# Performance work log

Measured on AMD Instinct MI355X. Metric: run time of the kernel, lower is better.

Reference implementation:

```python
import jax, jax.numpy as jnp
import numpy as np

E = 100000   # number of edges
S = 64       # multiplicity of 0e (scalar) irreps
V = 32       # multiplicity of 1o (vector) irreps; also number of gates
RS3 = 1.0 / np.sqrt(3.0)   # wigner_3j constant for (1,1,0)/(0,1,1)/(1,0,1) paths
RS6 = 1.0 / np.sqrt(6.0)   # (unused here: no 1o output from 1o x 1o)

# per-path normalization: 1/sqrt(n_paths_to_slot * mul1 * mul2), e3nn-style 'uvw'
A_SS_S = (2.0 * S * S) ** -0.5
A_VV_S = (2.0 * V * V) ** -0.5 * RS3
A_SS_G = (2.0 * S * S) ** -0.5
A_VV_G = (2.0 * V * V) ** -0.5 * RS3
A_SV_V = (2.0 * S * V) ** -0.5 * RS3
A_VS_V = (2.0 * V * S) ** -0.5 * RS3


def setup_inputs() -> dict:
    key = jax.random.key(0)
    ks = jax.random.split(key, 12)
    d_in = S + 3 * V
    return {
        "fea_in1": jax.random.normal(ks[0], (E, d_in), jnp.float32),
        "fea_in2": jax.random.normal(ks[1], (E, d_in), jnp.float32),
        "fea_weight": jax.random.normal(ks[2], (E, V), jnp.float32),   # unused (kept for signature parity)
        "batch_edge": jax.random.randint(ks[3], (E,), 0, 16, jnp.int32),  # unused (norm='')
        # SeparateWeightTensorProduct ('uvw') weights, one tensor per CG path
        "w_ss_s": jax.random.normal(ks[4], (S, S, S), jnp.float32),  # 0e x 0e -> 0e (scalars)
        "w_vv_s": jax.random.normal(ks[5], (V, V, S), jnp.float32),  # 1o x 1o -> 0e (scalars)
        "w_ss_g": jax.random.normal(ks[6], (S, S, V), jnp.float32),  # 0e x 0e -> 0e (gates)
        "w_vv_g": jax.random.normal(ks[7], (V, V, V), jnp.float32),  # 1o x 1o -> 0e (gates)
        "w_sv_v": jax.random.normal(ks[8], (S, V, V), jnp.float32),  # 0e x 1o -> 1o
        "w_vs_v": jax.random.normal(ks[9], (V, S, V), jnp.float32),  # 1o x 0e -> 1o
        # equivariant o3.Linear weights (channel mixing per irrep, shared over m)
        "wl_s": jax.random.normal(ks[10], (S, S), jnp.float32),
        "wl_v": jax.random.normal(ks[11], (V, V), jnp.float32),
    }


def reference(fea_in1, fea_in2, fea_weight, batch_edge,
              w_ss_s, w_vv_s, w_ss_g, w_vv_g, w_sv_v, w_vs_v, wl_s, wl_v):
    # split flattened irreps features: [S scalars | V vectors * 3]
    s1 = fea_in1[:, :S]
    v1 = fea_in1[:, S:].reshape(-1, V, 3)
    s2 = fea_in2[:, :S]
    v2 = fea_in2[:, S:].reshape(-1, V, 3)

    # --- separate-weight tensor product (fully connected 'uvw' paths) ---
    z_s = (A_SS_S * jnp.einsum('uvw,eu,ev->ew', w_ss_s, s1, s2)
           + A_VV_S * jnp.einsum('uvw,eui,evi->ew', w_vv_s, v1, v2))   # (E,S) 0e
    z_g = (A_SS_G * jnp.einsum('uvw,eu,ev->ew', w_ss_g, s1, s2)
           + A_VV_G * jnp.einsum('uvw,eui,evi->ew', w_vv_g, v1, v2))   # (E,V) gates 0e
    z_v = (A_SV_V * jnp.einsum('uvw,eu,evi->ewi', w_sv_v, s1, v2)
           + A_VS_V * jnp.einsum('uvw,eui,ev->ewi', w_vs_v, v1, s2))   # (E,V,3) 1o

    # --- gated nonlinearity: silu on scalars, sigmoid gates on vectors ---
    s_act = jax.nn.silu(z_s)
    v_act = jax.nn.sigmoid(z_g)[:, :, None] * z_v

    # --- equivariant linear (per-irrep channel mixing, fan-in normalized) ---
    s_out = (s_act @ wl_s) * (S ** -0.5)                    # (E,S)
    v_out = jnp.einsum('evi,vw->ewi', v_act, wl_v) * (V ** -0.5)  # (E,V,3)

    return jnp.concatenate([s_out, v_out.reshape(-1, 3 * V)], axis=-1)  # (E, S+3V)
```

## Files before the change

kernel.cpp:

```cpp
#include <hip/hip_runtime.h>


typedef _Float16 f16;
typedef _Float16 f16x4 __attribute__((ext_vector_type(4)));
typedef _Float16 f16x8 __attribute__((ext_vector_type(8)));
typedef float    f32x4 __attribute__((ext_vector_type(4)));

constexpr float A_SS  = 0.011048543456039806f;
constexpr float A_VV  = 0.012757759747374832f;
constexpr float A_SV  = 0.009021097956087904f;
constexpr float SO_SC = 0.125f;
constexpr float VO_SC = 0.1767766952966369f;

#define MFMA16(A, B, C) __builtin_amdgcn_mfma_f32_16x16x32_f16((A), (B), (C), 0, 0, 0)

static __device__ __forceinline__ f16x8 splat8(f16 x) {
    return (f16x8){x, x, x, x, x, x, x, x};
}

__global__ void prep_weights(const float* __restrict__ wss_s, const float* __restrict__ wvv_s,
                             const float* __restrict__ wss_g, const float* __restrict__ wvv_g,
                             const float* __restrict__ wsv,   const float* __restrict__ wvs,
                             const float* __restrict__ wls,   const float* __restrict__ wlv,
                             f16* __restrict__ b1p, f16* __restrict__ b2p,
                             f16* __restrict__ wlsP, f16* __restrict__ wlvP)
{
    int idx = blockIdx.x * 256 + threadIdx.x;
    const int N1 = 2 * 160 * 3 * 512;
    const int N2 = 128 * 2 * 512;
    const int N3 = 8 * 512;
    const int N4 = 2 * 512;
    if (idx < N1) {
        int j = idx & 7, L = (idx >> 3) & 63, rest = idx >> 9;
        int t3 = rest % 3, rc = rest / 3;
        int c = rc % 160, nh2 = rc / 160;
        int k = c * 32 + (L >> 4) * 8 + j;
        int n = (nh2 * 3 + t3) * 16 + (L & 15);
        float val;
        if (k < 4096) { int u = k >> 6, v = k & 63, p = u * 64 + v;
            val = A_SS * (n < 64 ? wss_s[p * 64 + n] : wss_g[p * 32 + (n - 64)]);
        } else { int k2 = k - 4096; int u = k2 >> 5, v = k2 & 31, p = u * 32 + v;
            val = A_VV * (n < 64 ? wvv_s[p * 64 + n] : wvv_g[p * 32 + (n - 64)]);
        }
        b1p[idx] = (f16)val;
    } else if (idx < N1 + N2) {
        int id2 = idx - N1;
        int j = id2 & 7, L = (id2 >> 3) & 63, ct = id2 >> 9;
        int t = ct & 1, c = ct >> 1;
        int k = c * 32 + (L >> 4) * 8 + j;
        int n = t * 16 + (L & 15);
        float val;
        if (k < 2048) { int u = k >> 5, v = k & 31; val = wsv[(u * 32 + v) * 32 + n]; }
        else { int k2 = k - 2048; int u = k2 >> 6, v = k2 & 63; val = wvs[(u * 64 + v) * 32 + n]; }
        b2p[id2] = (f16)(A_SV * val);
    } else if (idx < N1 + N2 + N3) {
        int id3 = idx - N1 - N2;
        int j = id3 & 7, L = (id3 >> 3) & 63, ct = id3 >> 9;
        int t = ct & 3, kc = ct >> 2;
        int k = kc * 32 + (L >> 4) * 8 + j;
        int n = t * 16 + (L & 15);
        wlsP[id3] = (f16)(SO_SC * wls[k * 64 + n]);
    } else if (idx < N1 + N2 + N3 + N4) {
        int id4 = idx - N1 - N2 - N3;
        int j = id4 & 7, L = (id4 >> 3) & 63, t = id4 >> 9;
        int k = (L >> 4) * 8 + j;
        int n = t * 16 + (L & 15);
        wlvP[id4] = (f16)(VO_SC * wlv[k * 32 + n]);
    }
}

__global__ __launch_bounds__(256, 4)
void seconv_mfma(const float* __restrict__ fea1, const float* __restrict__ fea2,
                 const f16* __restrict__ b1p, const f16* __restrict__ b2p,
                 const f16* __restrict__ wlsP, const f16* __restrict__ wlvP,
                 float* __restrict__ out, int E)
{
    __shared__ __align__(128) char smem[40960];
    f16*   zSh  = (f16*)smem;
    f16*   zGh  = (f16*)(smem + 9216);
    f16*   ZVH  = (f16*)(smem + 13568);
    float* OUTV = (float*)smem;

    const int tid  = threadIdx.x;
    const int lane = tid & 63;
    const int m    = lane & 15;
    const int quad = lane >> 4;
    const int w    = tid >> 6;
    const int h    = w & 1;
    const int nh   = w >> 1;
    const int tb   = nh * 3;
    const int e0   = blockIdx.x * 64;

    auto ld8 = [&](int e, int hc) -> f16x8 {
        int b = (e * 640 + hc * 2) ^ ((e & 7) << 4);
        return *(const f16x8*)(smem + b);
    };
    auto ld4 = [&](int e, int hc) -> f16x4 {
        int b = (e * 640 + hc * 2) ^ ((e & 7) << 4);
        return *(const f16x4*)(smem + b);
    };
    auto st2 = [&](int e, int hc, f16 v) {
        int b = (e * 640 + hc * 2) ^ ((e & 7) << 4);
        *(f16*)(smem + b) = v;
    };

    for (int i = tid; i < 64 * 160; i += 256) {
        int e = i / 160, c = i - e * 160;
        int ge = e0 + e; if (ge >= E) ge = E - 1;
        float a = fea1[ge * 160 + c];
        float b = fea2[ge * 160 + c];
        if (c < 64) { st2(e, c, (f16)a); st2(e, 64 + c, (f16)b); }
        else { int c2 = c - 64; int v = c2 / 3, ii = c2 - v * 3;
               st2(e, 128 + ii * 32 + v, (f16)a);
               st2(e, 224 + ii * 32 + v, (f16)b); }
    }
    __syncthreads();

    const int eA = h * 32 + m;
    const int eB = h * 32 + 16 + m;

    f32x4 acc[2][3];
    #pragma unroll
    for (int p = 0; p < 2; ++p)
        #pragma unroll
        for (int t = 0; t < 3; ++t) acc[p][t] = (f32x4){0.f, 0.f, 0.f, 0.f};

    const f16* pB = b1p + __builtin_amdgcn_readfirstlane(nh) * (160 * 3 * 512);
    f32x4 bq[2][3];
    #pragma unroll
    for (int t = 0; t < 3; ++t) bq[0][t] = *(const f32x4*)(pB + t * 512 + lane * 8);
    pB += 1536;
    #pragma unroll
    for (int t = 0; t < 3; ++t) bq[1][t] = *(const f32x4*)(pB + t * 512 + lane * 8);
    pB += 1536;

    {
        f16x8 s2q[2][2];
        #pragma unroll
        for (int p = 0; p < 2; ++p)
            #pragma unroll
            for (int vh = 0; vh < 2; ++vh)
                s2q[p][vh] = ld8(p ? eB : eA, 64 + vh * 32 + quad * 8);

        for (int ub = 0; ub < 8; ++ub) {
            f16x8 s1Ab = ld8(eA, ub * 8);
            f16x8 s1Bb = ld8(eB, ub * 8);
            #pragma unroll
            for (int uj = 0; uj < 8; ++uj) {
                f16x8 s1A = splat8(s1Ab[uj]);
                f16x8 s1B = splat8(s1Bb[uj]);
                #pragma unroll
                for (int vh = 0; vh < 2; ++vh) {
                    f16x8 bb0 = __builtin_bit_cast(f16x8, bq[vh][0]);
                    f16x8 bb1 = __builtin_bit_cast(f16x8, bq[vh][1]);
                    f16x8 bb2 = __builtin_bit_cast(f16x8, bq[vh][2]);
                    #pragma unroll
                    for (int t = 0; t < 3; ++t)
                        bq[vh][t] = *(const f32x4*)(pB + t * 512 + lane * 8);
                    pB += 1536;
                    f16x8 a0 = s1A * s2q[0][vh];
                    f16x8 a1 = s1B * s2q[1][vh];
                    acc[0][0] = MFMA16(a0, bb0, acc[0][0]);
                    acc[0][1] = MFMA16(a0, bb1, acc[0][1]);
                    acc[0][2] = MFMA16(a0, bb2, acc[0][2]);
                    acc[1][0] = MFMA16(a1, bb0, acc[1][0]);
                    acc[1][1] = MFMA16(a1, bb1, acc[1][1]);
                    acc[1][2] = MFMA16(a1, bb2, acc[1][2]);
                }
            }
        }
    }
    {
        f16x8 v2q[2][3];
        #pragma unroll
        for (int p = 0; p < 2; ++p)
            #pragma unroll
            for (int i3 = 0; i3 < 3; ++i3)
                v2q[p][i3] = ld8(p ? eB : eA, 224 + i3 * 32 + quad * 8);

        for (int ub = 0; ub < 8; ++ub) {
            f16x4 xA[3], xB[3];
            #pragma unroll
            for (int i3 = 0; i3 < 3; ++i3) {
                xA[i3] = ld4(eA, 128 + i3 * 32 + ub * 4);
                xB[i3] = ld4(eB, 128 + i3 * 32 + ub * 4);
            }
            #pragma unroll
            for (int uj = 0; uj < 4; ++uj) {
                const int slot = uj & 1;
                f16x8 bb0 = __builtin_bit_cast(f16x8, bq[slot][0]);
                f16x8 bb1 = __builtin_bit_cast(f16x8, bq[slot][1]);
                f16x8 bb2 = __builtin_bit_cast(f16x8, bq[slot][2]);
                #pragma unroll
                for (int t = 0; t < 3; ++t)
                    bq[slot][t] = *(const f32x4*)(pB + t * 512 + lane * 8);
                pB += 1536;
                f16x8 a0 = splat8(xA[0][uj]) * v2q[0][0];
                a0 += splat8(xA[1][uj]) * v2q[0][1];
                a0 += splat8(xA[2][uj]) * v2q[0][2];
                f16x8 a1 = splat8(xB[0][uj]) * v2q[1][0];
                a1 += splat8(xB[1][uj]) * v2q[1][1];
                a1 += splat8(xB[2][uj]) * v2q[1][2];
                acc[0][0] = MFMA16(a0, bb0, acc[0][0]);
                acc[0][1] = MFMA16(a0, bb1, acc[0][1]);
                acc[0][2] = MFMA16(a0, bb2, acc[0][2]);
                acc[1][0] = MFMA16(a1, bb0, acc[1][0]);
                acc[1][1] = MFMA16(a1, bb1, acc[1][1]);
                acc[1][2] = MFMA16(a1, bb2, acc[1][2]);
            }
        }
    }

    f16x4 zpk[2][3];
    #pragma unroll
    for (int p = 0; p < 2; ++p)
        #pragma unroll
        for (int t = 0; t < 3; ++t) {
            int n = (tb + t) * 16 + m;
            #pragma unroll
            for (int r = 0; r < 4; ++r) {
                float z = acc[p][t][r];
                float vv = (n < 64) ? (z / (1.f + __expf(-z))) : z;
                zpk[p][t][r] = (f16)vv;
            }
        }

    const int e2 = w * 16 + m;
    f16x8 s2g[2], v2g[3];
    #pragma unroll
    for (int vh = 0; vh < 2; ++vh)
        s2g[vh] = ld8(e2, 64 + vh * 32 + quad * 8);
    #pragma unroll
    for (int i3 = 0; i3 < 3; ++i3)
        v2g[i3] = ld8(e2, 224 + i3 * 32 + quad * 8);

    f32x4 acc2[3][2];
    #pragma unroll
    for (int i3 = 0; i3 < 3; ++i3)
        #pragma unroll
        for (int t = 0; t < 2; ++t) acc2[i3][t] = (f32x4){0.f, 0.f, 0.f, 0.f};

    const f16* pB2 = b2p;
    f32x4 bq2[2][2];
    #pragma unroll
    for (int t = 0; t < 2; ++t) bq2[0][t] = *(const f32x4*)(pB2 + t * 512 + lane * 8);
    pB2 += 1024;
    #pragma unroll
    for (int t = 0; t < 2; ++t) bq2[1][t] = *(const f32x4*)(pB2 + t * 512 + lane * 8);
    pB2 += 1024;

    for (int ub = 0; ub < 8; ++ub) {
        f16x8 s1b = ld8(e2, ub * 8);
        #pragma unroll
        for (int uj = 0; uj < 8; ++uj) {
            const int slot = uj & 1;
            f16x8 bb0 = __builtin_bit_cast(f16x8, bq2[slot][0]);
            f16x8 bb1 = __builtin_bit_cast(f16x8, bq2[slot][1]);
            #pragma unroll
            for (int t = 0; t < 2; ++t)
                bq2[slot][t] = *(const f32x4*)(pB2 + t * 512 + lane * 8);
            pB2 += 1024;
            f16x8 sxv = splat8(s1b[uj]);
            #pragma unroll
            for (int i3 = 0; i3 < 3; ++i3) {
                f16x8 a = sxv * v2g[i3];
                acc2[i3][0] = MFMA16(a, bb0, acc2[i3][0]);
                acc2[i3][1] = MFMA16(a, bb1, acc2[i3][1]);
            }
        }
    }
    for (int ub = 0; ub < 4; ++ub) {
        f16x8 v1b[3];
        #pragma unroll
        for (int i3 = 0; i3 < 3; ++i3)
            v1b[i3] = ld8(e2, 128 + i3 * 32 + ub * 8);
        #pragma unroll
        for (int uj = 0; uj < 8; ++uj) {
            f16x8 v1s0 = splat8(v1b[0][uj]);
            f16x8 v1s1 = splat8(v1b[1][uj]);
            f16x8 v1s2 = splat8(v1b[2][uj]);
            #pragma unroll
            for (int vh = 0; vh < 2; ++vh) {
                const int slot = vh;
                f16x8 bb0 = __builtin_bit_cast(f16x8, bq2[slot][0]);
                f16x8 bb1 = __builtin_bit_cast(f16x8, bq2[slot][1]);
                #pragma unroll
                for (int t = 0; t < 2; ++t)
                    bq2[slot][t] = *(const f32x4*)(pB2 + t * 512 + lane * 8);
                pB2 += 1024;
                f16x8 a0 = v1s0 * s2g[vh];
                f16x8 a1 = v1s1 * s2g[vh];
                f16x8 a2 = v1s2 * s2g[vh];
                acc2[0][0] = MFMA16(a0, bb0, acc2[0][0]);
                acc2[0][1] = MFMA16(a0, bb1, acc2[0][1]);
                acc2[1][0] = MFMA16(a1, bb0, acc2[1][0]);
                acc2[1][1] = MFMA16(a1, bb1, acc2[1][1]);
                acc2[2][0] = MFMA16(a2, bb0, acc2[2][0]);
                acc2[2][1] = MFMA16(a2, bb1, acc2[2][1]);
            }
        }
    }
    __syncthreads();

    #pragma unroll
    for (int p = 0; p < 2; ++p)
        #pragma unroll
        for (int t = 0; t < 3; ++t) {
            int n = (tb + t) * 16 + m;
            #pragma unroll
            for (int r = 0; r < 4; ++r) {
                int e_loc = h * 32 + p * 16 + quad * 4 + r;
                if (n < 64) zSh[e_loc * 72 + n] = zpk[p][t][r];
                else        zGh[e_loc * 34 + (n - 64)] = zpk[p][t][r];
            }
        }
    __syncthreads();

    #pragma unroll
    for (int t = 0; t < 2; ++t)
        #pragma unroll
        for (int r = 0; r < 4; ++r) {
            int e_loc = w * 16 + quad * 4 + r;
            float zg = (float)zGh[e_loc * 34 + t * 16 + m];
            float gate = 1.f / (1.f + __expf(-zg));
            #pragma unroll
            for (int i3 = 0; i3 < 3; ++i3)
                ZVH[(i3 * 64 + e_loc) * 40 + t * 16 + m] = (f16)(gate * acc2[i3][t][r]);
        }

    {
        f32x4 accS[4];
        #pragma unroll
        for (int t = 0; t < 4; ++t) accS[t] = (f32x4){0.f, 0.f, 0.f, 0.f};
        #pragma unroll
        for (int kc = 0; kc < 2; ++kc) {
            f16x8 aS = *(const f16x8*)(zSh + (w * 16 + m) * 72 + kc * 32 + quad * 8);
            #pragma unroll
            for (int t = 0; t < 4; ++t) {
                f32x4 braw = *(const f32x4*)(wlsP + ((kc * 4 + t) * 64 + lane) * 8);
                accS[t] = MFMA16(aS, __builtin_bit_cast(f16x8, braw), accS[t]);
            }
        }
        #pragma unroll
        for (int t = 0; t < 4; ++t)
            #pragma unroll
            for (int r = 0; r < 4; ++r) {
                int ge = e0 + w * 16 + quad * 4 + r;
                if (ge < E) out[ge * 160 + t * 16 + m] = accS[t][r];
            }
    }
    {
        f32x4 accV[3][2];
        #pragma unroll
        for (int i3 = 0; i3 < 3; ++i3)
            #pragma unroll
            for (int t = 0; t < 2; ++t) accV[i3][t] = (f32x4){0.f, 0.f, 0.f, 0.f};
        f16x8 bV[2];
        #pragma unroll
        for (int t = 0; t < 2; ++t) {
            f32x4 braw = *(const f32x4*)(wlvP + (t * 64 + lane) * 8);
            bV[t] = __builtin_bit_cast(f16x8, braw);
        }
        #pragma unroll
        for (int i3 = 0; i3 < 3; ++i3) {
            f16x8 aV = *(const f16x8*)(ZVH + (i3 * 64 + w * 16 + m) * 40 + quad * 8);
            #pragma unroll
            for (int t = 0; t < 2; ++t) accV[i3][t] = MFMA16(aV, bV[t], accV[i3][t]);
        }
        __syncthreads();
        #pragma unroll
        for (int i3 = 0; i3 < 3; ++i3)
            #pragma unroll
            for (int t = 0; t < 2; ++t)
                #pragma unroll
                for (int r = 0; r < 4; ++r) {
                    int e_loc = w * 16 + quad * 4 + r;
                    OUTV[e_loc * 100 + (t * 16 + m) * 3 + i3] = accV[i3][t][r];
                }
    }
    __syncthreads();

    for (int i = tid; i < 64 * 96; i += 256) {
        int e = i / 96, c = i - e * 96;
        int ge = e0 + e;
        if (ge < E) out[ge * 160 + 64 + c] = OUTV[e * 100 + c];
    }
}

extern "C" void kernel_launch(void* const* d_in, const int* in_sizes, int n_in,
                              void* d_out, int out_size, void* d_ws, size_t ws_size,
                              hipStream_t stream) {
    const float* fea1  = (const float*)d_in[0];
    const float* fea2  = (const float*)d_in[1];
    const float* wss_s = (const float*)d_in[4];
    const float* wvv_s = (const float*)d_in[5];
    const float* wss_g = (const float*)d_in[6];
    const float* wvv_g = (const float*)d_in[7];
    const float* wsv   = (const float*)d_in[8];
    const float* wvs   = (const float*)d_in[9];
    const float* wls   = (const float*)d_in[10];
    const float* wlv   = (const float*)d_in[11];
    float* out = (float*)d_out;

    f16* b1p  = (f16*)d_ws;
    f16* b2p  = (f16*)((char*)d_ws + 983040);
    f16* wlsP = (f16*)((char*)d_ws + 1245184);
    f16* wlvP = (f16*)((char*)d_ws + 1253376);

    int E = in_sizes[0] / 160;
    int prep_total = 491520 + 131072 + 4096 + 1024;
    prep_weights<<<dim3((prep_total + 255) / 256), dim3(256), 0, stream>>>(
        wss_s, wvv_s, wss_g, wvv_g, wsv, wvs, wls, wlv, b1p, b2p, wlsP, wlvP);
    int grid = (E + 63) / 64;
    seconv_mfma<<<dim3(grid), dim3(256), 0, stream>>>(
        fea1, fea2, b1p, b2p, wlsP, wlvP, out, E);
}
```

Baseline: 396.7 us.

## Vectorize input staging loads and stagger per-wave weight streaming start offsets

The shared-memory staging loop now reads float4 chunks of each edge row and writes packed f16 pairs for the scalar parts, replacing scalar per-element global loads. The first tensor-product loop and the s×v loop now start at a wave-dependent u-block offset and wrap around. Waves that share a weight slice therefore read different parts of the weight stream at the same time, which spreads cache and L2 traffic. The cost is more code from the duplicated loop bodies and extra prefetch prologues.

```diff
diff --git a/kernel.cpp b/kernel.cpp
--- a/kernel.cpp
+++ b/kernel.cpp
@@ -2,6 +2,7 @@
 
 
 typedef _Float16 f16;
+typedef _Float16 f16x2 __attribute__((ext_vector_type(2)));
 typedef _Float16 f16x4 __attribute__((ext_vector_type(4)));
 typedef _Float16 f16x8 __attribute__((ext_vector_type(8)));
 typedef float    f32x4 __attribute__((ext_vector_type(4)));
@@ -103,16 +104,33 @@
         int b = (e * 640 + hc * 2) ^ ((e & 7) << 4);
         *(f16*)(smem + b) = v;
     };
-
-    for (int i = tid; i < 64 * 160; i += 256) {
-        int e = i / 160, c = i - e * 160;
+    auto stp = [&](int e, int hc, f16x2 v) {
+        int b = (e * 640 + hc * 2) ^ ((e & 7) << 4);
+        *(f16x2*)(smem + b) = v;
+    };
+
+    for (int i = tid; i < 64 * 40; i += 256) {
+        int e = i / 40, g = i - e * 40;
         int ge = e0 + e; if (ge >= E) ge = E - 1;
-        float a = fea1[ge * 160 + c];
-        float b = fea2[ge * 160 + c];
-        if (c < 64) { st2(e, c, (f16)a); st2(e, 64 + c, (f16)b); }
-        else { int c2 = c - 64; int v = c2 / 3, ii = c2 - v * 3;
-               st2(e, 128 + ii * 32 + v, (f16)a);
-               st2(e, 224 + ii * 32 + v, (f16)b); }
+        float4 a4 = *(const float4*)(fea1 + ge * 160 + g * 4);
+        float4 b4 = *(const float4*)(fea2 + ge * 160 + g * 4);
+        if (g < 16) {
+            int c = g * 4;
+            stp(e, c,        (f16x2){(f16)a4.x, (f16)a4.y});
+            stp(e, c + 2,    (f16x2){(f16)a4.z, (f16)a4.w});
+            stp(e, 64 + c,   (f16x2){(f16)b4.x, (f16)b4.y});
+            stp(e, 64 + c + 2, (f16x2){(f16)b4.z, (f16)b4.w});
+        } else {
+            float av[4] = {a4.x, a4.y, a4.z, a4.w};
+            float bv[4] = {b4.x, b4.y, b4.z, b4.w};
+            #pragma unroll
+            for (int k = 0; k < 4; ++k) {
+                int cc = g * 4 - 64 + k;
+                int v = cc / 3, ii = cc - v * 3;
+                st2(e, 128 + ii * 32 + v, (f16)av[k]);
+                st2(e, 224 + ii * 32 + v, (f16)bv[k]);
+            }
+        }
     }
     __syncthreads();
 
@@ -125,14 +143,8 @@
         #pragma unroll
         for (int t = 0; t < 3; ++t) acc[p][t] = (f32x4){0.f, 0.f, 0.f, 0.f};
 
-    const f16* pB = b1p + __builtin_amdgcn_readfirstlane(nh) * (160 * 3 * 512);
+    const f16* pBs = b1p + __builtin_amdgcn_readfirstlane(nh) * (160 * 3 * 512);
     f32x4 bq[2][3];
-    #pragma unroll
-    for (int t = 0; t < 3; ++t) bq[0][t] = *(const f32x4*)(pB + t * 512 + lane * 8);
-    pB += 1536;
-    #pragma unroll
-    for (int t = 0; t < 3; ++t) bq[1][t] = *(const f32x4*)(pB + t * 512 + lane * 8);
-    pB += 1536;
 
     {
         f16x8 s2q[2][2];
@@ -142,33 +154,45 @@
             for (int vh = 0; vh < 2; ++vh)
                 s2q[p][vh] = ld8(p ? eB : eA, 64 + vh * 32 + quad * 8);
 
-        for (int ub = 0; ub < 8; ++ub) {
-            f16x8 s1Ab = ld8(eA, ub * 8);
-            f16x8 s1Bb = ld8(eB, ub * 8);
-            #pragma unroll
-            for (int uj = 0; uj < 8; ++uj) {
-                f16x8 s1A = splat8(s1Ab[uj]);
-                f16x8 s1B = splat8(s1Bb[uj]);
+        auto runP = [&](int ubb, int ube) {
+            const f16* p = pBs + ubb * (16 * 1536);
+            #pragma unroll
+            for (int t = 0; t < 3; ++t) bq[0][t] = *(const f32x4*)(p + t * 512 + lane * 8);
+            p += 1536;
+            #pragma unroll
+            for (int t = 0; t < 3; ++t) bq[1][t] = *(const f32x4*)(p + t * 512 + lane * 8);
+            p += 1536;
+            for (int ub = ubb; ub < ube; ++ub) {
+                f16x8 s1Ab = ld8(eA, ub * 8);
+                f16x8 s1Bb = ld8(eB, ub * 8);
                 #pragma unroll
-                for (int vh = 0; vh < 2; ++vh) {
-                    f16x8 bb0 = __builtin_bit_cast(f16x8, bq[vh][0]);
-                    f16x8 bb1 = __builtin_bit_cast(f16x8, bq[vh][1]);
-                    f16x8 bb2 = __builtin_bit_cast(f16x8, bq[vh][2]);
+                for (int uj = 0; uj < 8; ++uj) {
+                    f16x8 s1A = splat8(s1Ab[uj]);
+                    f16x8 s1B = splat8(s1Bb[uj]);
                     #pragma unroll
-                    for (int t = 0; t < 3; ++t)
-                        bq[vh][t] = *(const f32x4*)(pB + t * 512 + lane * 8);
-                    pB += 1536;
-                    f16x8 a0 = s1A * s2q[0][vh];
-                    f16x8 a1 = s1B * s2q[1][vh];
-                    acc[0][0] = MFMA16(a0, bb0, acc[0][0]);
-                    acc[0][1] = MFMA16(a0, bb1, acc[0][1]);
-                    acc[0][2] = MFMA16(a0, bb2, acc[0][2]);
-                    acc[1][0] = MFMA16(a1, bb0, acc[1][0]);
-                    acc[1][1] = MFMA16(a1, bb1, acc[1][1]);
-                    acc[1][2] = MFMA16(a1, bb2, acc[1][2]);
+                    for (int vh = 0; vh < 2; ++vh) {
+                        f16x8 bb0 = __builtin_bit_cast(f16x8, bq[vh][0]);
+                        f16x8 bb1 = __builtin_bit_cast(f16x8, bq[vh][1]);
+                        f16x8 bb2 = __builtin_bit_cast(f16x8, bq[vh][2]);
+                        #pragma unroll
+                        for (int t = 0; t < 3; ++t)
+                            bq[vh][t] = *(const f32x4*)(p + t * 512 + lane * 8);
+                        p += 1536;
+                        f16x8 a0 = s1A * s2q[0][vh];
+                        f16x8 a1 = s1B * s2q[1][vh];
+                        acc[0][0] = MFMA16(a0, bb0, acc[0][0]);
+                        acc[0][1] = MFMA16(a0, bb1, acc[0][1]);
+                        acc[0][2] = MFMA16(a0, bb2, acc[0][2]);
+                        acc[1][0] = MFMA16(a1, bb0, acc[1][0]);
+                        acc[1][1] = MFMA16(a1, bb1, acc[1][1]);
+                        acc[1][2] = MFMA16(a1, bb2, acc[1][2]);
+                    }
                 }
             }
-        }
+        };
+        const int off = h * 4;
+        runP(off, 8);
+        if (off) runP(0, off);
     }
     {
         f16x8 v2q[2][3];
@@ -178,6 +202,13 @@
             for (int i3 = 0; i3 < 3; ++i3)
                 v2q[p][i3] = ld8(p ? eB : eA, 224 + i3 * 32 + quad * 8);
 
+        const f16* p = pBs + 128 * 1536;
+        #pragma unroll
+        for (int t = 0; t < 3; ++t) bq[0][t] = *(const f32x4*)(p + t * 512 + lane * 8);
+        p += 1536;
+        #pragma unroll
+        for (int t = 0; t < 3; ++t) bq[1][t] = *(const f32x4*)(p + t * 512 + lane * 8);
+        p += 1536;
         for (int ub = 0; ub < 8; ++ub) {
             f16x4 xA[3], xB[3];
             #pragma unroll
@@ -193,8 +224,8 @@
                 f16x8 bb2 = __builtin_bit_cast(f16x8, bq[slot][2]);
                 #pragma unroll
                 for (int t = 0; t < 3; ++t)
-                    bq[slot][t] = *(const f32x4*)(pB + t * 512 + lane * 8);
-                pB += 1536;
+                    bq[slot][t] = *(const f32x4*)(p + t * 512 + lane * 8);
+                p += 1536;
                 f16x8 a0 = splat8(xA[0][uj]) * v2q[0][0];
                 a0 += splat8(xA[1][uj]) * v2q[0][1];
                 a0 += splat8(xA[2][uj]) * v2q[0][2];
@@ -240,63 +271,79 @@
         #pragma unroll
         for (int t = 0; t < 2; ++t) acc2[i3][t] = (f32x4){0.f, 0.f, 0.f, 0.f};
 
-    const f16* pB2 = b2p;
     f32x4 bq2[2][2];
-    #pragma unroll
-    for (int t = 0; t < 2; ++t) bq2[0][t] = *(const f32x4*)(pB2 + t * 512 + lane * 8);
-    pB2 += 1024;
-    #pragma unroll
-    for (int t = 0; t < 2; ++t) bq2[1][t] = *(const f32x4*)(pB2 + t * 512 + lane * 8);
-    pB2 += 1024;
-
-    for (int ub = 0; ub < 8; ++ub) {
-        f16x8 s1b = ld8(e2, ub * 8);
-        #pragma unroll
-        for (int uj = 0; uj < 8; ++uj) {
-            const int slot = uj & 1;
-            f16x8 bb0 = __builtin_bit_cast(f16x8, bq2[slot][0]);
-            f16x8 bb1 = __builtin_bit_cast(f16x8, bq2[slot][1]);
-            #pragma unroll
-            for (int t = 0; t < 2; ++t)
-                bq2[slot][t] = *(const f32x4*)(pB2 + t * 512 + lane * 8);
-            pB2 += 1024;
-            f16x8 sxv = splat8(s1b[uj]);
-            #pragma unroll
-            for (int i3 = 0; i3 < 3; ++i3) {
-                f16x8 a = sxv * v2g[i3];
-                acc2[i3][0] = MFMA16(a, bb0, acc2[i3][0]);
-                acc2[i3][1] = MFMA16(a, bb1, acc2[i3][1]);
-            }
-        }
-    }
-    for (int ub = 0; ub < 4; ++ub) {
-        f16x8 v1b[3];
-        #pragma unroll
-        for (int i3 = 0; i3 < 3; ++i3)
-            v1b[i3] = ld8(e2, 128 + i3 * 32 + ub * 8);
-        #pragma unroll
-        for (int uj = 0; uj < 8; ++uj) {
-            f16x8 v1s0 = splat8(v1b[0][uj]);
-            f16x8 v1s1 = splat8(v1b[1][uj]);
-            f16x8 v1s2 = splat8(v1b[2][uj]);
-            #pragma unroll
-            for (int vh = 0; vh < 2; ++vh) {
-                const int slot = vh;
-                f16x8 bb0 = __builtin_bit_cast(f16x8, bq2[slot][0]);
-                f16x8 bb1 = __builtin_bit_cast(f16x8, bq2[slot][1]);
+
+    {
+        auto runSV = [&](int ubb, int ube) {
+            const f16* p = b2p + ubb * (8 * 1024);
+            #pragma unroll
+            for (int t = 0; t < 2; ++t) bq2[0][t] = *(const f32x4*)(p + t * 512 + lane * 8);
+            p += 1024;
+            #pragma unroll
+            for (int t = 0; t < 2; ++t) bq2[1][t] = *(const f32x4*)(p + t * 512 + lane * 8);
+            p += 1024;
+            for (int ub = ubb; ub < ube; ++ub) {
+                f16x8 s1b = ld8(e2, ub * 8);
                 #pragma unroll
-                for (int t = 0; t < 2; ++t)
-                    bq2[slot][t] = *(const f32x4*)(pB2 + t * 512 + lane * 8);
-                pB2 += 1024;
-                f16x8 a0 = v1s0 * s2g[vh];
-                f16x8 a1 = v1s1 * s2g[vh];
-                f16x8 a2 = v1s2 * s2g[vh];
-                acc2[0][0] = MFMA16(a0, bb0, acc2[0][0]);
-                acc2[0][1] = MFMA16(a0, bb1, acc2[0][1]);
-                acc2[1][0] = MFMA16(a1, bb0, acc2[1][0]);
-                acc2[1][1] = MFMA16(a1, bb1, acc2[1][1]);
-                acc2[2][0] = MFMA16(a2, bb0, acc2[2][0]);
-                acc2[2][1] = MFMA16(a2, bb1, acc2[2][1]);
+                for (int uj = 0; uj < 8; ++uj) {
+                    const int slot = uj & 1;
+                    f16x8 bb0 = __builtin_bit_cast(f16x8, bq2[slot][0]);
+                    f16x8 bb1 = __builtin_bit_cast(f16x8, bq2[slot][1]);
+                    #pragma unroll
+                    for (int t = 0; t < 2; ++t)
+                        bq2[slot][t] = *(const f32x4*)(p + t * 512 + lane * 8);
+                    p += 1024;
+                    f16x8 sxv = splat8(s1b[uj]);
+                    #pragma unroll
+                    for (int i3 = 0; i3 < 3; ++i3) {
+                        f16x8 a = sxv * v2g[i3];
+                        acc2[i3][0] = MFMA16(a, bb0, acc2[i3][0]);
+                        acc2[i3][1] = MFMA16(a, bb1, acc2[i3][1]);
+                    }
+                }
+            }
+        };
+        const int off2 = w * 2;
+        runSV(off2, 8);
+        if (off2) runSV(0, off2);
+    }
+    {
+        const f16* p = b2p + 64 * 1024;
+        #pragma unroll
+        for (int t = 0; t < 2; ++t) bq2[0][t] = *(const f32x4*)(p + t * 512 + lane * 8);
+        p += 1024;
+        #pragma unroll
+        for (int t = 0; t < 2; ++t) bq2[1][t] = *(const f32x4*)(p + t * 512 + lane * 8);
+        p += 1024;
+        for (int ub = 0; ub < 4; ++ub) {
+            f16x8 v1b[3];
+            #pragma unroll
+            for (int i3 = 0; i3 < 3; ++i3)
+                v1b[i3] = ld8(e2, 128 + i3 * 32 + ub * 8);
+            #pragma unroll
+            for (int uj = 0; uj < 8; ++uj) {
+                f16x8 v1s0 = splat8(v1b[0][uj]);
+                f16x8 v1s1 = splat8(v1b[1][uj]);
+                f16x8 v1s2 = splat8(v1b[2][uj]);
+                #pragma unroll
+                for (int vh = 0; vh < 2; ++vh) {
+                    const int slot = vh;
+                    f16x8 bb0 = __builtin_bit_cast(f16x8, bq2[slot][0]);
+                    f16x8 bb1 = __builtin_bit_cast(f16x8, bq2[slot][1]);
+                    #pragma unroll
+                    for (int t = 0; t < 2; ++t)
+                        bq2[slot][t] = *(const f32x4*)(p + t * 512 + lane * 8);
+                    p += 1024;
+                    f16x8 a0 = v1s0 * s2g[vh];
+                    f16x8 a1 = v1s1 * s2g[vh];
+                    f16x8 a2 = v1s2 * s2g[vh];
+                    acc2[0][0] = MFMA16(a0, bb0, acc2[0][0]);
+                    acc2[0][1] = MFMA16(a0, bb1, acc2[0][1]);
+                    acc2[1][0] = MFMA16(a1, bb0, acc2[1][0]);
+                    acc2[1][1] = MFMA16(a1, bb1, acc2[1][1]);
+                    acc2[2][0] = MFMA16(a2, bb0, acc2[2][0]);
+                    acc2[2][1] = MFMA16(a2, bb1, acc2[2][1]);
+                }
             }
         }
     }
```

After: 397.2 us. Within noise of the previous version (+0.1%).
